# Performance work log

Hardware: AMD Instinct MI355X
Metric: run time of the kernel (lower is better)

## Reference

```python
import jax, jax.numpy as jnp
import numpy as np
from jax import lax

B, T, E, H = 32, 512, 256, 512

def setup_inputs() -> dict:
    key = jax.random.key(0)
    ks = jax.random.split(key, 7)
    s = 1.0 / np.sqrt(H)  # PyTorch RNN init range
    u = lambda k, sh: jax.random.uniform(k, sh, jnp.float32, -s, s)
    return {
        "xs": jax.random.normal(ks[0], (B, T, E), jnp.float32),
        "w_ih0": u(ks[1], (2, H, E)),      # [dir, H, in]
        "w_hh0": u(ks[2], (2, H, H)),
        "b0":    u(ks[3], (2, 2, H)),      # [dir, (b_ih,b_hh), H]
        "w_ih1": u(ks[4], (2, H, 2 * H)),
        "w_hh1": u(ks[5], (2, H, H)),
        "b1":    u(ks[6], (2, 2, H)),
    }

def _rnn_dir(x_tbi, w_ih, w_hh, b_ih, b_hh, reverse):
    # Precompute the input GEMM for all timesteps: [T,B,H]
    pre = jnp.einsum('tbi,hi->tbh', x_tbi, w_ih) + b_ih + b_hh
    h0 = jnp.zeros((x_tbi.shape[1], w_hh.shape[0]), x_tbi.dtype)
    def step(h, p):
        h = jnp.tanh(p + h @ w_hh.T)
        return h, h
    _, hs = lax.scan(step, h0, pre, reverse=reverse)  # ys aligned with xs order
    hy = hs[0] if reverse else hs[-1]
    return hs, hy

def _layer(x_tbi, w_ih, w_hh, b):
    hf, hyf = _rnn_dir(x_tbi, w_ih[0], w_hh[0], b[0, 0], b[0, 1], False)
    hb, hyb = _rnn_dir(x_tbi, w_ih[1], w_hh[1], b[1, 0], b[1, 1], True)
    return jnp.concatenate([hf, hb], axis=-1), jnp.stack([hyf, hyb])

def reference(xs, w_ih0, w_hh0, b0, w_ih1, w_hh1, b1):
    x = jnp.transpose(xs, (1, 0, 2))          # batch_first -> [T,B,E]
    h1, hy0 = _layer(x, w_ih0, w_hh0, b0)     # [T,B,2H], [2,B,H]
    h2, hy1 = _layer(h1, w_ih1, w_hh1, b1)
    hs = jnp.transpose(h2, (1, 0, 2))         # [B,T,2H]
    hy = jnp.concatenate([hy0, hy1], axis=0)  # [4,B,H] layer-major like PyTorch
    # F.dropout with p=0.0 is identity
    return (hs, hy)
```

## Files before the change

kernel.cpp:

```cpp
#include <hip/hip_runtime.h>
#include <hip/hip_fp16.h>


#define T_ 512
#define B_ 32
#define E_ 256
#define H_ 512

using half8 = _Float16 __attribute__((ext_vector_type(8)));
using f32x4 = float __attribute__((ext_vector_type(4)));
typedef unsigned long long u64;
typedef unsigned int u32;

static constexpr size_t OFF_PRE   = 0;
static constexpr size_t OFF_XH1   = 32ull << 20;
static constexpr size_t OFF_X0H   = 64ull << 20;
static constexpr size_t OFF_W0H   = 72ull << 20;
static constexpr size_t OFF_W1H   = OFF_W0H + (512ull << 10);
static constexpr size_t OFF_WHH   = OFF_W1H + (2ull << 20);
static constexpr size_t OFF_BS    = OFF_WHH + (2ull << 20);
static constexpr size_t OFF_HX    = OFF_BS + (8ull << 10);
static constexpr size_t ZERO_SIZE = 512ull << 10;

__device__ __forceinline__ float fast_tanh(float x) {
    float cx = fminf(fmaxf(x, -9.0f), 9.0f);
    float e2 = __expf(2.0f * cx);
    return (e2 - 1.0f) * __builtin_amdgcn_rcpf(e2 + 1.0f);
}

__global__ void prep_kernel(const float* __restrict__ xs,
                            const float* __restrict__ wih0,
                            const float* __restrict__ whh0,
                            const float* __restrict__ b0,
                            const float* __restrict__ wih1,
                            const float* __restrict__ whh1,
                            const float* __restrict__ b1,
                            _Float16* __restrict__ x0h,
                            _Float16* __restrict__ w0h,
                            _Float16* __restrict__ w1h,
                            _Float16* __restrict__ whh,
                            float* __restrict__ bsum)
{
    const int N0 = T_ * B_ * E_;
    const int N1 = 2 * H_ * E_;
    const int N2 = 2 * H_ * 2*H_;
    const int N3 = 2 * H_ * H_;
    const int total = N0 + N1 + N2 + 2 * N3 + 2048;
    for (int idx = blockIdx.x * blockDim.x + threadIdx.x; idx < total;
         idx += gridDim.x * blockDim.x) {
        int i = idx;
        if (i < N0) {
            int t = i >> 13;
            int r = i & 8191;
            int b = r >> 8;
            int e = r & 255;
            x0h[i] = (_Float16)xs[((size_t)(b << 9) + t) * 256 + e];
        } else if ((i -= N0) < N1) {
            w0h[i] = (_Float16)wih0[i];
        } else if ((i -= N1) < N2) {
            w1h[i] = (_Float16)wih1[i];
        } else if ((i -= N2) < N3) {
            whh[i] = (_Float16)whh0[i];
        } else if ((i -= N3) < N3) {
            whh[N3 + i] = (_Float16)whh1[i];
        } else {
            i -= N3;
            int layer = i >> 10;
            int r = i & 1023;
            int d = r >> 9;
            int j = r & 511;
            const float* bb = layer ? b1 : b0;
            bsum[i] = bb[d * 1024 + j] + bb[d * 1024 + 512 + j];
        }
    }
}

__global__ __launch_bounds__(256, 2)
void gemm_kernel(const _Float16* __restrict__ X,
                 const _Float16* __restrict__ W,
                 const float* __restrict__ bias,
                 _Float16* __restrict__ out, int K)
{
    __shared__ _Float16 Ash[64][72];
    __shared__ _Float16 Bsh[64][72];
    const int m0 = blockIdx.x * 64, n0 = blockIdx.y * 64, d = blockIdx.z;
    const _Float16* Wd = W + (size_t)d * 512 * K;
    const int tid = threadIdx.x;
    const int l = tid & 63, w = tid >> 6;
    const int wm = w & 1, wn = w >> 1;
    const int lm = l & 15, q = l >> 4;
    f32x4 c[2][2] = {};
    for (int kk = 0; kk < K; kk += 64) {
        for (int ci = tid; ci < 512; ci += 256) {
            int row = ci >> 3, col = (ci & 7) * 8;
            *(half8*)&Ash[row][col] =
                *(const half8*)&X[(size_t)(m0 + row) * K + kk + col];
            *(half8*)&Bsh[row][col] =
                *(const half8*)&Wd[(size_t)(n0 + row) * K + kk + col];
        }
        __syncthreads();
        for (int kt = 0; kt < 2; ++kt) {
            const int kof = kt * 32 + q * 8;
            half8 a0 = *(const half8*)&Ash[wm * 32 + lm][kof];
            half8 a1 = *(const half8*)&Ash[wm * 32 + 16 + lm][kof];
            half8 b0f = *(const half8*)&Bsh[wn * 32 + lm][kof];
            half8 b1f = *(const half8*)&Bsh[wn * 32 + 16 + lm][kof];
            c[0][0] = __builtin_amdgcn_mfma_f32_16x16x32_f16(a0, b0f, c[0][0], 0, 0, 0);
            c[0][1] = __builtin_amdgcn_mfma_f32_16x16x32_f16(a0, b1f, c[0][1], 0, 0, 0);
            c[1][0] = __builtin_amdgcn_mfma_f32_16x16x32_f16(a1, b0f, c[1][0], 0, 0, 0);
            c[1][1] = __builtin_amdgcn_mfma_f32_16x16x32_f16(a1, b1f, c[1][1], 0, 0, 0);
        }
        __syncthreads();
    }
    _Float16* outd = out + (size_t)d * 16384 * 512;
    for (int mi = 0; mi < 2; ++mi)
        for (int ni = 0; ni < 2; ++ni) {
            int col = n0 + wn * 32 + ni * 16 + lm;
            float bv = bias[d * 512 + col];
            for (int r = 0; r < 4; ++r) {
                int rowm = m0 + wm * 32 + mi * 16 + q * 4 + r;
                outd[(size_t)rowm * 512 + col] = (_Float16)(c[mi][ni][r] + bv);
            }
        }
}

__global__ __launch_bounds__(256)
void rnn_kernel(const _Float16* __restrict__ pre,
                const _Float16* __restrict__ whh,
                u64* __restrict__ hx,
                _Float16* __restrict__ xh1,
                float* __restrict__ dout,
                int layer)
{
    __shared__ uint4 As[64 * 33];
    const int gid = blockIdx.x;
    const int d = gid >> 4, g = gid & 15;
    const int tid = threadIdx.x, wv = tid >> 6, l = tid & 63;
    const int lm = l & 15, q = l >> 4;
    const int wm = wv & 1, wn = wv >> 1;
    const int jn = g * 32 + wn * 16;
    const int bA = wm * 16 + lm;
    const int bq = wm * 16 + q * 4;

    half8 Bf[16];
    {
        const _Float16* wrow = whh + ((size_t)d * 512 + jn + lm) * 512;
#pragma unroll
        for (int kt = 0; kt < 16; ++kt)
            Bf[kt] = *(const half8*)&wrow[kt * 32 + q * 8];
    }

    u64* hbd = hx + (size_t)d * 2 * 8192;
    const int jp_pub = (jn + (lm & ~1)) >> 1;
    const int scat_base = ((tid >> 2) * 33) * 4 + (tid & 3);
    u32* AsW = (u32*)As;

    for (int s = 0; s < T_; ++s) {
        const int t = d ? (T_ - 1 - s) : s;

        const _Float16* prow = pre + ((size_t)d * 16384 + (size_t)t * B_) * 512 + jn + lm;
        _Float16 pv[4];
#pragma unroll
        for (int r = 0; r < 4; ++r)
            pv[r] = prow[(size_t)(bq + r) * 512];

        const u64* src = hbd + (size_t)(s & 1) * 8192 + tid;
        const unsigned tag = (unsigned)s;
        u64 wvv[32];
        bool stale = true;
        do {
#pragma unroll
            for (int i = 0; i < 32; ++i)
                wvv[i] = __hip_atomic_load(&src[i * 256],
                                           __ATOMIC_RELAXED, __HIP_MEMORY_SCOPE_SYSTEM);
            bool ok = true;
#pragma unroll
            for (int i = 0; i < 32; ++i)
                ok &= ((unsigned)(wvv[i] >> 32) == tag);
            stale = __any(!ok);
        } while (stale);

        __syncthreads();
#pragma unroll
        for (int i = 0; i < 32; ++i)
            AsW[scat_base + i * 4] = (u32)wvv[i];
        __syncthreads();

        f32x4 c0, c1;
#pragma unroll
        for (int r = 0; r < 4; ++r) { c0[r] = (float)pv[r]; c1[r] = 0.0f; }
#pragma unroll
        for (int kt = 0; kt < 16; ++kt) {
            union { uint4 u; half8 h; } cv;
            cv.u = As[(kt * 4 + q) * 33 + bA];
            if (kt & 1) c1 = __builtin_amdgcn_mfma_f32_16x16x32_f16(cv.h, Bf[kt], c1, 0, 0, 0);
            else        c0 = __builtin_amdgcn_mfma_f32_16x16x32_f16(cv.h, Bf[kt], c0, 0, 0, 0);
        }

        u64* dst = hbd + (size_t)((s + 1) & 1) * 8192;
        const u64 tagw = ((u64)(unsigned)(s + 1)) << 32;
        const int j = jn + lm;
        float hv[4];
        unsigned hb[4];
#pragma unroll
        for (int r = 0; r < 4; ++r) {
            hv[r] = fast_tanh(c0[r] + c1[r]);
            union { _Float16 f; unsigned short u; } cb;
            cb.f = (_Float16)hv[r];
            hb[r] = cb.u;
        }
#pragma unroll
        for (int r = 0; r < 4; ++r) {
            unsigned p = __shfl_xor(hb[r], 1, 64);
            unsigned lo = (l & 1) ? p : hb[r];
            unsigned hi = (l & 1) ? hb[r] : p;
            if ((r >> 1) == (l & 1)) {
                u64 word = tagw | ((u64)hi << 16) | lo;
                __hip_atomic_store(&dst[(size_t)(bq + r) * 256 + jp_pub], word,
                                   __ATOMIC_RELAXED, __HIP_MEMORY_SCOPE_SYSTEM);
            }
        }
#pragma unroll
        for (int r = 0; r < 4; ++r) {
            const int b = bq + r;
            if (layer == 0) {
                xh1[((size_t)t * B_ + b) * 1024 + d * 512 + j] = (_Float16)hv[r];
            } else {
                dout[((size_t)b * T_ + t) * 1024 + d * 512 + j] = hv[r];
            }
            if (s == T_ - 1) {
                dout[16777216ull + ((size_t)(layer * 2 + d) * B_ + b) * 512 + j] = hv[r];
            }
        }
    }
}

extern "C" void kernel_launch(void* const* d_in, const int* in_sizes, int n_in,
                              void* d_out, int out_size, void* d_ws, size_t ws_size,
                              hipStream_t stream)
{
    const float* xs   = (const float*)d_in[0];
    const float* wih0 = (const float*)d_in[1];
    const float* whh0 = (const float*)d_in[2];
    const float* b0   = (const float*)d_in[3];
    const float* wih1 = (const float*)d_in[4];
    const float* whh1 = (const float*)d_in[5];
    const float* b1   = (const float*)d_in[6];

    char* ws = (char*)d_ws;
    _Float16* pre  = (_Float16*)(ws + OFF_PRE);
    _Float16* xh1  = (_Float16*)(ws + OFF_XH1);
    _Float16* x0h  = (_Float16*)(ws + OFF_X0H);
    _Float16* w0h  = (_Float16*)(ws + OFF_W0H);
    _Float16* w1h  = (_Float16*)(ws + OFF_W1H);
    _Float16* whh  = (_Float16*)(ws + OFF_WHH);
    float*    bsum = (float*)(ws + OFF_BS);
    u64*      hx   = (u64*)(ws + OFF_HX);
    float*    out  = (float*)d_out;

    (void)hipMemsetAsync(ws + OFF_HX, 0, ZERO_SIZE, stream);

    prep_kernel<<<2048, 256, 0, stream>>>(xs, wih0, whh0, b0, wih1, whh1, b1,
                                          x0h, w0h, w1h, whh, bsum);

    gemm_kernel<<<dim3(256, 8, 2), 256, 0, stream>>>(x0h, w0h, bsum, pre, 256);
    rnn_kernel<<<32, 256, 0, stream>>>(pre, whh, hx, xh1, out, 0);

    gemm_kernel<<<dim3(256, 8, 2), 256, 0, stream>>>(xh1, w1h, bsum + 1024, pre, 1024);
    rnn_kernel<<<32, 256, 0, stream>>>(pre, whh + 2 * 512 * 512,
                                       hx + 2 * 2 * 8192, xh1, out, 1);
}
```

Before: 2.894 ms.

## Split each RNN direction across two large blocks with overlapped own-half compute

Reworks the recurrent kernel so each direction uses two 512-thread blocks, each owning half the hidden units and keeping its own half of the state in shared memory. Only the peer half is exchanged through tagged global atomics. The own-half MFMA contribution is issued before polling for the peer's data, so the work overlaps the wait. This reduces cross-block synchronization fan-in and polling traffic, at the cost of much more per-block compute on far fewer CUs and higher register pressure from holding twice the weight fragments.

```diff
diff --git a/kernel.cpp b/kernel.cpp
--- a/kernel.cpp
+++ b/kernel.cpp
@@ -124,7 +124,7 @@
         }
 }
 
-__global__ __launch_bounds__(256)
+__global__ __launch_bounds__(512, 2)
 void rnn_kernel(const _Float16* __restrict__ pre,
                 const _Float16* __restrict__ whh,
                 u64* __restrict__ hx,
@@ -133,105 +133,151 @@
                 int layer)
 {
     __shared__ uint4 As[64 * 33];
-    const int gid = blockIdx.x;
-    const int d = gid >> 4, g = gid & 15;
-    const int tid = threadIdx.x, wv = tid >> 6, l = tid & 63;
+    const int bi = blockIdx.x;
+    const int d = bi >> 1, half = bi & 1, peer = half ^ 1;
+    const int tid = threadIdx.x, w = tid >> 6, l = tid & 63;
     const int lm = l & 15, q = l >> 4;
-    const int wm = wv & 1, wn = wv >> 1;
-    const int jn = g * 32 + wn * 16;
-    const int bA = wm * 16 + lm;
-    const int bq = wm * 16 + q * 4;
-
-    half8 Bf[16];
-    {
-        const _Float16* wrow = whh + ((size_t)d * 512 + jn + lm) * 512;
+    const int jw = half * 256 + w * 32;
+
+    half8 Bf[2][16];
+#pragma unroll
+    for (int nt = 0; nt < 2; ++nt) {
+        const _Float16* wrow = whh + ((size_t)d * 512 + jw + nt * 16 + lm) * 512;
 #pragma unroll
         for (int kt = 0; kt < 16; ++kt)
-            Bf[kt] = *(const half8*)&wrow[kt * 32 + q * 8];
+            Bf[nt][kt] = *(const half8*)&wrow[kt * 32 + q * 8];
     }
 
-    u64* hbd = hx + (size_t)d * 2 * 8192;
-    const int jp_pub = (jn + (lm & ~1)) >> 1;
-    const int scat_base = ((tid >> 2) * 33) * 4 + (tid & 3);
+    u64* hdir = hx + (size_t)d * 16384;
     u32* AsW = (u32*)As;
+    const int om0 = half * 8;
+    const int pm0 = peer * 8;
+
+    for (int i = tid; i < 1024; i += 512)
+        As[(half * 32 + (i >> 5)) * 33 + (i & 31)] = uint4{0, 0, 0, 0};
+    __syncthreads();
 
     for (int s = 0; s < T_; ++s) {
         const int t = d ? (T_ - 1 - s) : s;
-
-        const _Float16* prow = pre + ((size_t)d * 16384 + (size_t)t * B_) * 512 + jn + lm;
-        _Float16 pv[4];
-#pragma unroll
-        for (int r = 0; r < 4; ++r)
-            pv[r] = prow[(size_t)(bq + r) * 512];
-
-        const u64* src = hbd + (size_t)(s & 1) * 8192 + tid;
+        const int p = s & 1;
+
+        const u64* src = hdir + (size_t)p * 8192 + (size_t)peer * 4096 + tid;
+        u64 w8[8];
+#pragma unroll
+        for (int i = 0; i < 8; ++i)
+            w8[i] = __hip_atomic_load(&src[i * 512],
+                                      __ATOMIC_RELAXED, __HIP_MEMORY_SCOPE_SYSTEM);
+
+        const _Float16* prow = pre + ((size_t)d * 16384 + (size_t)t * B_) * 512 + jw;
+        _Float16 pv[2][2][4];
+#pragma unroll
+        for (int m = 0; m < 2; ++m)
+#pragma unroll
+            for (int nt = 0; nt < 2; ++nt)
+#pragma unroll
+                for (int r = 0; r < 4; ++r)
+                    pv[m][nt][r] = prow[(size_t)(m * 16 + q * 4 + r) * 512 + nt * 16 + lm];
+
+        f32x4 acc[2][2] = {};
+#pragma unroll
+        for (int kk = 0; kk < 8; ++kk) {
+            const int kt = om0 + kk;
+            union { uint4 u; half8 h; } a0, a1;
+            a0.u = As[(kt * 4 + q) * 33 + lm];
+            a1.u = As[(kt * 4 + q) * 33 + 16 + lm];
+            acc[0][0] = __builtin_amdgcn_mfma_f32_16x16x32_f16(a0.h, Bf[0][kt], acc[0][0], 0, 0, 0);
+            acc[0][1] = __builtin_amdgcn_mfma_f32_16x16x32_f16(a0.h, Bf[1][kt], acc[0][1], 0, 0, 0);
+            acc[1][0] = __builtin_amdgcn_mfma_f32_16x16x32_f16(a1.h, Bf[0][kt], acc[1][0], 0, 0, 0);
+            acc[1][1] = __builtin_amdgcn_mfma_f32_16x16x32_f16(a1.h, Bf[1][kt], acc[1][1], 0, 0, 0);
+        }
+
         const unsigned tag = (unsigned)s;
-        u64 wvv[32];
-        bool stale = true;
-        do {
-#pragma unroll
-            for (int i = 0; i < 32; ++i)
-                wvv[i] = __hip_atomic_load(&src[i * 256],
+        for (;;) {
+            bool ok = true;
+#pragma unroll
+            for (int i = 0; i < 8; ++i)
+                ok &= ((unsigned)(w8[i] >> 32) == tag);
+            if (!__any(!ok)) break;
+#pragma unroll
+            for (int i = 0; i < 8; ++i)
+                w8[i] = __hip_atomic_load(&src[i * 512],
+                                          __ATOMIC_RELAXED, __HIP_MEMORY_SCOPE_SYSTEM);
+        }
+
+#pragma unroll
+        for (int i = 0; i < 8; ++i) {
+            const int wi = i * 512 + tid;
+            const int b = wi >> 7, jpl = wi & 127;
+            const int jpg = peer * 128 + jpl;
+            AsW[((jpg >> 2) * 33 + b) * 4 + (jpg & 3)] = (u32)w8[i];
+        }
+        __syncthreads();
+
+#pragma unroll
+        for (int kk = 0; kk < 8; ++kk) {
+            const int kt = pm0 + kk;
+            union { uint4 u; half8 h; } a0, a1;
+            a0.u = As[(kt * 4 + q) * 33 + lm];
+            a1.u = As[(kt * 4 + q) * 33 + 16 + lm];
+            acc[0][0] = __builtin_amdgcn_mfma_f32_16x16x32_f16(a0.h, Bf[0][kt], acc[0][0], 0, 0, 0);
+            acc[0][1] = __builtin_amdgcn_mfma_f32_16x16x32_f16(a0.h, Bf[1][kt], acc[0][1], 0, 0, 0);
+            acc[1][0] = __builtin_amdgcn_mfma_f32_16x16x32_f16(a1.h, Bf[0][kt], acc[1][0], 0, 0, 0);
+            acc[1][1] = __builtin_amdgcn_mfma_f32_16x16x32_f16(a1.h, Bf[1][kt], acc[1][1], 0, 0, 0);
+        }
+
+        u64* dst = hdir + (size_t)(p ^ 1) * 8192 + (size_t)half * 4096;
+        const u64 tagw = ((u64)(unsigned)(s + 1)) << 32;
+        float hvf[2][2][4];
+#pragma unroll
+        for (int m = 0; m < 2; ++m)
+#pragma unroll
+            for (int nt = 0; nt < 2; ++nt) {
+                unsigned hb[4];
+#pragma unroll
+                for (int r = 0; r < 4; ++r) {
+                    const float hv = fast_tanh(acc[m][nt][r] + (float)pv[m][nt][r]);
+                    hvf[m][nt][r] = hv;
+                    union { _Float16 f; unsigned short u; } cb;
+                    cb.f = (_Float16)hv;
+                    hb[r] = cb.u;
+                }
+#pragma unroll
+                for (int r = 0; r < 4; ++r) {
+                    const unsigned ps = __shfl_xor(hb[r], 1, 64);
+                    const unsigned lo = (l & 1) ? ps : hb[r];
+                    const unsigned hi = (l & 1) ? hb[r] : ps;
+                    if ((r >> 1) == (l & 1)) {
+                        const int b = m * 16 + q * 4 + r;
+                        const int jpl = (w * 32 + nt * 16 + (lm & ~1)) >> 1;
+                        const u64 word = tagw | ((u64)hi << 16) | lo;
+                        __hip_atomic_store(&dst[b * 128 + jpl], word,
                                            __ATOMIC_RELAXED, __HIP_MEMORY_SCOPE_SYSTEM);
-            bool ok = true;
-#pragma unroll
-            for (int i = 0; i < 32; ++i)
-                ok &= ((unsigned)(wvv[i] >> 32) == tag);
-            stale = __any(!ok);
-        } while (stale);
+                        const int jpg = half * 128 + jpl;
+                        AsW[((jpg >> 2) * 33 + b) * 4 + (jpg & 3)] = (u32)word;
+                    }
+                }
+            }
+
+#pragma unroll
+        for (int m = 0; m < 2; ++m)
+#pragma unroll
+            for (int nt = 0; nt < 2; ++nt)
+#pragma unroll
+                for (int r = 0; r < 4; ++r) {
+                    const int b = m * 16 + q * 4 + r;
+                    const int j = jw + nt * 16 + lm;
+                    const float hv = hvf[m][nt][r];
+                    if (layer == 0) {
+                        xh1[((size_t)t * B_ + b) * 1024 + d * 512 + j] = (_Float16)hv;
+                    } else {
+                        dout[((size_t)b * T_ + t) * 1024 + d * 512 + j] = hv;
+                    }
+                    if (s == T_ - 1) {
+                        dout[16777216ull + ((size_t)(layer * 2 + d) * B_ + b) * 512 + j] = hv;
+                    }
+                }
 
         __syncthreads();
-#pragma unroll
-        for (int i = 0; i < 32; ++i)
-            AsW[scat_base + i * 4] = (u32)wvv[i];
-        __syncthreads();
-
-        f32x4 c0, c1;
-#pragma unroll
-        for (int r = 0; r < 4; ++r) { c0[r] = (float)pv[r]; c1[r] = 0.0f; }
-#pragma unroll
-        for (int kt = 0; kt < 16; ++kt) {
-            union { uint4 u; half8 h; } cv;
-            cv.u = As[(kt * 4 + q) * 33 + bA];
-            if (kt & 1) c1 = __builtin_amdgcn_mfma_f32_16x16x32_f16(cv.h, Bf[kt], c1, 0, 0, 0);
-            else        c0 = __builtin_amdgcn_mfma_f32_16x16x32_f16(cv.h, Bf[kt], c0, 0, 0, 0);
-        }
-
-        u64* dst = hbd + (size_t)((s + 1) & 1) * 8192;
-        const u64 tagw = ((u64)(unsigned)(s + 1)) << 32;
-        const int j = jn + lm;
-        float hv[4];
-        unsigned hb[4];
-#pragma unroll
-        for (int r = 0; r < 4; ++r) {
-            hv[r] = fast_tanh(c0[r] + c1[r]);
-            union { _Float16 f; unsigned short u; } cb;
-            cb.f = (_Float16)hv[r];
-            hb[r] = cb.u;
-        }
-#pragma unroll
-        for (int r = 0; r < 4; ++r) {
-            unsigned p = __shfl_xor(hb[r], 1, 64);
-            unsigned lo = (l & 1) ? p : hb[r];
-            unsigned hi = (l & 1) ? hb[r] : p;
-            if ((r >> 1) == (l & 1)) {
-                u64 word = tagw | ((u64)hi << 16) | lo;
-                __hip_atomic_store(&dst[(size_t)(bq + r) * 256 + jp_pub], word,
-                                   __ATOMIC_RELAXED, __HIP_MEMORY_SCOPE_SYSTEM);
-            }
-        }
-#pragma unroll
-        for (int r = 0; r < 4; ++r) {
-            const int b = bq + r;
-            if (layer == 0) {
-                xh1[((size_t)t * B_ + b) * 1024 + d * 512 + j] = (_Float16)hv[r];
-            } else {
-                dout[((size_t)b * T_ + t) * 1024 + d * 512 + j] = hv[r];
-            }
-            if (s == T_ - 1) {
-                dout[16777216ull + ((size_t)(layer * 2 + d) * B_ + b) * 512 + j] = hv[r];
-            }
-        }
     }
 }
 
@@ -264,9 +310,9 @@
                                           x0h, w0h, w1h, whh, bsum);
 
     gemm_kernel<<<dim3(256, 8, 2), 256, 0, stream>>>(x0h, w0h, bsum, pre, 256);
-    rnn_kernel<<<32, 256, 0, stream>>>(pre, whh, hx, xh1, out, 0);
+    rnn_kernel<<<4, 512, 0, stream>>>(pre, whh, hx, xh1, out, 0);
 
     gemm_kernel<<<dim3(256, 8, 2), 256, 0, stream>>>(xh1, w1h, bsum + 1024, pre, 1024);
-    rnn_kernel<<<32, 256, 0, stream>>>(pre, whh + 2 * 512 * 512,
-                                       hx + 2 * 2 * 8192, xh1, out, 1);
-}
+    rnn_kernel<<<4, 512, 0, stream>>>(pre, whh + 2 * 512 * 512,
+                                      hx + 2 * 16384, xh1, out, 1);
+}
```

Result: slower. 11.10 ms (+283.7%).
